# Optimization experiments

Hardware: AMD Instinct MI355X
Metric: run time of the kernel (lower is better)

## Reference

```python
import jax, jax.numpy as jnp
import numpy as np

B, SQ, SKV, H, D = 4, 128, 8192, 32, 128


def setup_inputs() -> dict:
    key = jax.random.key(0)
    k1, k2, k3 = jax.random.split(key, 3)
    q = jax.random.normal(k1, (B, SQ, H, D), dtype=jnp.float32)
    k = jax.random.normal(k2, (B, SKV, H, D), dtype=jnp.float32)
    v = jax.random.normal(k3, (B, SKV, H, D), dtype=jnp.float32)
    return {"q": q, "k": k, "v": v}


def reference(q, k, v):
    # Full (non-causal) multi-head decode attention with softmax scale 1/sqrt(D).
    # The kernel computes this via split-KV online softmax + LSE combine;
    # mathematically it equals standard softmax attention over all KV.
    scale = 1.0 / np.sqrt(q.shape[-1]).astype(np.float32)
    # scores: [B, H, SQ, SKV]
    scores = jnp.einsum("bqhd,bkhd->bhqk", q, k) * scale
    probs = jax.nn.softmax(scores, axis=-1)
    out = jnp.einsum("bhqk,bkhd->bqhd", probs, v)
    return out
```

## Files before the change

### kernel.cpp

```cpp
#include <hip/hip_runtime.h>
#include <hip/hip_bf16.h>
#include <cstdint>

#define B_ 4
#define SQ_ 128
#define SKV_ 8192
#define H_ 32
#define D_ 128
#define KT 32
#define HD (H_ * D_)

typedef __bf16 bf16x8 __attribute__((ext_vector_type(8)));
typedef float f32x4 __attribute__((ext_vector_type(4)));

union U4B8 { uint4 u; bf16x8 v; };

__device__ inline unsigned f2b_pack(float a, float b){
  unsigned ua = __float_as_uint(a); ua = (ua + 0x7FFFu + ((ua >> 16) & 1u)) >> 16;
  unsigned ub = __float_as_uint(b); ub = (ub + 0x7FFFu + ((ub >> 16) & 1u)) >> 16;
  return (ua & 0xFFFFu) | (ub << 16);
}
__device__ inline unsigned short f2b1(float a){
  unsigned ua = __float_as_uint(a);
  return (unsigned short)((ua + 0x7FFFu + ((ua >> 16) & 1u)) >> 16);
}

__global__ __launch_bounds__(512, 4) void mha_split_kernel(
    const float* __restrict__ q, const float* __restrict__ k, const float* __restrict__ v,
    float* __restrict__ Ubase, float* __restrict__ Lbase, float* __restrict__ outp, int nsplit)
{
  __shared__ char smem[40 * 1024] __attribute__((aligned(16)));

  const int tid = threadIdx.x;
  const int w = tid >> 6;
  const int l = tid & 63;
  const int g = l >> 4;
  const int c = l & 15;
  char* Plds = smem + 32768 + w * 1024;

  const int bh = blockIdx.x;
  const int split = blockIdx.y;
  const int b = bh >> 5, h = bh & 31;
  const int kps = SKV_ / nsplit;
  const int kv0 = split * kps;
  const int nt = kps / KT;

  const float qscale = 0.08838834764831845f * 1.4426950408889634f;

  bf16x8 qf[4];
  {
    const float* qr = q + (((size_t)b * SQ_ + (w * 16 + c)) * H_ + h) * D_;
#pragma unroll
    for (int ks = 0; ks < 4; ++ks) {
      int d0 = ks * 32 + g * 8;
      float4 x = *(const float4*)(qr + d0);
      float4 y = *(const float4*)(qr + d0 + 4);
      U4B8 t;
      t.u.x = f2b_pack(x.x * qscale, x.y * qscale);
      t.u.y = f2b_pack(x.z * qscale, x.w * qscale);
      t.u.z = f2b_pack(y.x * qscale, y.y * qscale);
      t.u.w = f2b_pack(y.z * qscale, y.w * qscale);
      qf[ks] = t.v;
    }
  }

  f32x4 oacc[8];
#pragma unroll
  for (int ni = 0; ni < 8; ++ni) oacc[ni] = (f32x4)0.0f;
  float lacc[4] = {};

  const float* kbase = k + ((size_t)b * SKV_ + kv0) * HD + (size_t)h * D_;
  const float* vbase = v + ((size_t)b * SKV_ + kv0) * HD + (size_t)h * D_;

  const int key_s = tid >> 4;
  const int d8_s  = (tid & 15) * 8;
  const int kp_s  = tid >> 5;
  const int d4_s  = (tid & 31) * 4;
  const int koff_w = key_s * 256 + ((d8_s * 2) ^ ((key_s & 7) << 4));

  float4 kreg0, kreg1, vreg0, vreg1;

  {
    const float* kt = kbase + (size_t)key_s * HD + d8_s;
    kreg0 = *(const float4*)(kt);
    kreg1 = *(const float4*)(kt + 4);
    const float* vt = vbase + (size_t)(kp_s * 2) * HD + d4_s;
    vreg0 = *(const float4*)(vt);
    vreg1 = *(const float4*)(vt + HD);
    uint4 kw;
    kw.x = f2b_pack(kreg0.x, kreg0.y); kw.y = f2b_pack(kreg0.z, kreg0.w);
    kw.z = f2b_pack(kreg1.x, kreg1.y); kw.w = f2b_pack(kreg1.z, kreg1.w);
    *(uint4*)(smem + koff_w) = kw;
    float va[4] = {vreg0.x, vreg0.y, vreg0.z, vreg0.w};
    float vb[4] = {vreg1.x, vreg1.y, vreg1.z, vreg1.w};
#pragma unroll
    for (int i = 0; i < 4; ++i) {
      int d = d4_s + i;
      int slot = ((kp_s >> 2) ^ ((d >> 2) & 3)) & 3;
      *(unsigned*)(smem + 16384 + d * 64 + slot * 16 + (kp_s & 3) * 4) = f2b_pack(va[i], vb[i]);
    }
  }
  __syncthreads();

  for (int t = 0; t < nt; ++t) {
    const int cur = t & 1;
    char* kc = smem + cur * 8192;
    char* vc = smem + 16384 + cur * 8192;

    if (t + 1 < nt) {
      const float* kt = kbase + (size_t)(t + 1) * KT * HD + (size_t)key_s * HD + d8_s;
      kreg0 = *(const float4*)(kt);
      kreg1 = *(const float4*)(kt + 4);
      const float* vt = vbase + (size_t)(t + 1) * KT * HD + (size_t)(kp_s * 2) * HD + d4_s;
      vreg0 = *(const float4*)(vt);
      vreg1 = *(const float4*)(vt + HD);
    }
    __builtin_amdgcn_sched_barrier(0);

    __builtin_amdgcn_s_setprio(1);
    f32x4 sacc[2];
#pragma unroll
    for (int ni = 0; ni < 2; ++ni) sacc[ni] = (f32x4)0.0f;
#pragma unroll
    for (int ni = 0; ni < 2; ++ni) {
      int key = ni * 16 + c;
      int rb = key * 256;
      int sw = (key & 7) << 4;
#pragma unroll
      for (int ks = 0; ks < 4; ++ks) {
        U4B8 bf;
        bf.u = *(uint4*)(kc + rb + ((ks * 64 + g * 16) ^ sw));
        sacc[ni] = __builtin_amdgcn_mfma_f32_16x16x32_bf16(qf[ks], bf.v, sacc[ni], 0, 0, 0);
      }
    }

#pragma unroll
    for (int ni = 0; ni < 2; ++ni) {
#pragma unroll
      for (int r = 0; r < 4; ++r) {
        float p = exp2f(sacc[ni][r]);
        lacc[r] += p;
        int row = g * 4 + r;
        int col = ni * 16 + c;
        int off = row * 64 + ((((col >> 3) ^ g) & 3) * 16) + (col & 7) * 2;
        *(unsigned short*)(Plds + off) = f2b1(p);
      }
    }

    {
      const int slot = ((g ^ (c >> 2)) & 3) * 16;
      U4B8 ap;
      ap.u = *(uint4*)(Plds + c * 64 + slot);
#pragma unroll
      for (int ni = 0; ni < 8; ++ni) {
        int d = ni * 16 + c;
        U4B8 bv;
        bv.u = *(uint4*)(vc + d * 64 + slot);
        oacc[ni] = __builtin_amdgcn_mfma_f32_16x16x32_bf16(ap.v, bv.v, oacc[ni], 0, 0, 0);
      }
    }
    __builtin_amdgcn_s_setprio(0);

    if (t + 1 < nt) {
      char* kn = smem + (cur ^ 1) * 8192;
      char* vn = smem + 16384 + (cur ^ 1) * 8192;
      uint4 kw;
      kw.x = f2b_pack(kreg0.x, kreg0.y); kw.y = f2b_pack(kreg0.z, kreg0.w);
      kw.z = f2b_pack(kreg1.x, kreg1.y); kw.w = f2b_pack(kreg1.z, kreg1.w);
      *(uint4*)(kn + koff_w) = kw;
      float va[4] = {vreg0.x, vreg0.y, vreg0.z, vreg0.w};
      float vb[4] = {vreg1.x, vreg1.y, vreg1.z, vreg1.w};
#pragma unroll
      for (int i = 0; i < 4; ++i) {
        int d = d4_s + i;
        int slot = ((kp_s >> 2) ^ ((d >> 2) & 3)) & 3;
        *(unsigned*)(vn + d * 64 + slot * 16 + (kp_s & 3) * 4) = f2b_pack(va[i], vb[i]);
      }
    }
    __syncthreads();
  }

#pragma unroll
  for (int r = 0; r < 4; ++r) {
    float s = lacc[r];
    s += __shfl_xor(s, 1, 16);
    s += __shfl_xor(s, 2, 16);
    s += __shfl_xor(s, 4, 16);
    s += __shfl_xor(s, 8, 16);
    lacc[r] = s;
  }

  if (nsplit == 1) {
    float* op = outp + (((size_t)b * SQ_) * H_ + h) * D_;
#pragma unroll
    for (int r = 0; r < 4; ++r) {
      int row = w * 16 + g * 4 + r;
      float inv = 1.0f / lacc[r];
#pragma unroll
      for (int ni = 0; ni < 8; ++ni) {
        op[(size_t)row * HD + ni * 16 + c] = oacc[ni][r] * inv;
      }
    }
  } else {
    float* Up = Ubase + ((size_t)split * 128 + bh) * (SQ_ * D_);
#pragma unroll
    for (int r = 0; r < 4; ++r) {
      int row = w * 16 + g * 4 + r;
#pragma unroll
      for (int ni = 0; ni < 8; ++ni) {
        Up[(size_t)row * D_ + ni * 16 + c] = oacc[ni][r];
      }
      if (c == 0) Lbase[((size_t)split * 128 + bh) * SQ_ + row] = lacc[r];
    }
  }
}

__global__ void mha_combine_kernel(const float* __restrict__ Ubase, const float* __restrict__ Lbase,
                                   float* __restrict__ outp, int nsplit) {
  int idx = blockIdx.x * 256 + threadIdx.x;
  int rowlin = idx >> 7;
  int d = idx & 127;
  float su = 0.f, sl = 0.f;
  for (int s = 0; s < nsplit; ++s) {
    su += Ubase[(size_t)s * (128 * SQ_ * D_) + idx];
    sl += Lbase[(size_t)s * (128 * SQ_) + rowlin];
  }
  int bh = rowlin >> 7, row = rowlin & 127;
  int b = bh >> 5, h = bh & 31;
  outp[(((size_t)b * SQ_ + row) * H_ + h) * D_ + d] = su / sl;
}

extern "C" void kernel_launch(void* const* d_in, const int* in_sizes, int n_in,
                              void* d_out, int out_size, void* d_ws, size_t ws_size,
                              hipStream_t stream) {
  const float* q = (const float*)d_in[0];
  const float* k = (const float*)d_in[1];
  const float* v = (const float*)d_in[2];
  float* outp = (float*)d_out;

  const size_t per_split = (size_t)128 * SQ_ * D_ * 4 + (size_t)128 * SQ_ * 4;
  int nsplit = 1;
  if (ws_size >= 4 * per_split) nsplit = 4;
  else if (ws_size >= 2 * per_split) nsplit = 2;

  float* Ubase = (float*)d_ws;
  float* Lbase = Ubase + (size_t)nsplit * 128 * SQ_ * D_;

  dim3 grid(128, nsplit);
  mha_split_kernel<<<grid, 512, 0, stream>>>(q, k, v, Ubase, Lbase, outp, nsplit);
  if (nsplit > 1) {
    mha_combine_kernel<<<(128 * SQ_ * D_) / 256, 256, 0, stream>>>(Ubase, Lbase, outp, nsplit);
  }
}
```

Measured before the change: 198.0 us.

## Deepen KV prefetch to two tiles ahead with unrolled ping-pong loop

Unrolls the KV tile loop by two and keeps two register sets of prefetched K/V, so global loads for tile t+2 are issued while tile t is computed, giving more latency hiding. Launch bounds minimum blocks per CU drops from 4 to 2 to allow the extra registers. It trades fewer resident waves (lower occupancy) for deeper software prefetch.

```diff
diff --git a/kernel.cpp b/kernel.cpp
--- a/kernel.cpp
+++ b/kernel.cpp
@@ -25,7 +25,7 @@
   return (unsigned short)((ua + 0x7FFFu + ((ua >> 16) & 1u)) >> 16);
 }
 
-__global__ __launch_bounds__(512, 4) void mha_split_kernel(
+__global__ __launch_bounds__(512, 2) void mha_split_kernel(
     const float* __restrict__ q, const float* __restrict__ k, const float* __restrict__ v,
     float* __restrict__ Ubase, float* __restrict__ Lbase, float* __restrict__ outp, int nsplit)
 {
@@ -78,107 +78,103 @@
   const int d4_s  = (tid & 31) * 4;
   const int koff_w = key_s * 256 + ((d8_s * 2) ^ ((key_s & 7) << 4));
 
-  float4 kreg0, kreg1, vreg0, vreg1;
-
-  {
-    const float* kt = kbase + (size_t)key_s * HD + d8_s;
-    kreg0 = *(const float4*)(kt);
-    kreg1 = *(const float4*)(kt + 4);
-    const float* vt = vbase + (size_t)(kp_s * 2) * HD + d4_s;
-    vreg0 = *(const float4*)(vt);
-    vreg1 = *(const float4*)(vt + HD);
-    uint4 kw;
-    kw.x = f2b_pack(kreg0.x, kreg0.y); kw.y = f2b_pack(kreg0.z, kreg0.w);
-    kw.z = f2b_pack(kreg1.x, kreg1.y); kw.w = f2b_pack(kreg1.z, kreg1.w);
-    *(uint4*)(smem + koff_w) = kw;
-    float va[4] = {vreg0.x, vreg0.y, vreg0.z, vreg0.w};
-    float vb[4] = {vreg1.x, vreg1.y, vreg1.z, vreg1.w};
-#pragma unroll
-    for (int i = 0; i < 4; ++i) {
-      int d = d4_s + i;
-      int slot = ((kp_s >> 2) ^ ((d >> 2) & 3)) & 3;
-      *(unsigned*)(smem + 16384 + d * 64 + slot * 16 + (kp_s & 3) * 4) = f2b_pack(va[i], vb[i]);
-    }
-  }
+  float4 kA0, kA1, vA0, vA1;
+  float4 kB0, kB1, vB0, vB1;
+
+#define ISSUE(T, K0r, K1r, V0r, V1r)                                          \
+  {                                                                           \
+    const float* kt_ = kbase + (size_t)(T) * KT * HD + (size_t)key_s * HD + d8_s; \
+    K0r = *(const float4*)(kt_);                                              \
+    K1r = *(const float4*)(kt_ + 4);                                          \
+    const float* vt_ = vbase + (size_t)(T) * KT * HD + (size_t)(kp_s * 2) * HD + d4_s; \
+    V0r = *(const float4*)(vt_);                                              \
+    V1r = *(const float4*)(vt_ + HD);                                         \
+  }
+
+#define WRITE_LDS(KDST, VDST, K0r, K1r, V0r, V1r)                             \
+  {                                                                           \
+    uint4 kw_;                                                                \
+    kw_.x = f2b_pack(K0r.x, K0r.y); kw_.y = f2b_pack(K0r.z, K0r.w);           \
+    kw_.z = f2b_pack(K1r.x, K1r.y); kw_.w = f2b_pack(K1r.z, K1r.w);           \
+    *(uint4*)((KDST) + koff_w) = kw_;                                         \
+    float va0_ = V0r.x, va1_ = V0r.y, va2_ = V0r.z, va3_ = V0r.w;             \
+    float vb0_ = V1r.x, vb1_ = V1r.y, vb2_ = V1r.z, vb3_ = V1r.w;             \
+    int d0_ = d4_s;                                                           \
+    int slotbase_ = (kp_s >> 2);                                              \
+    int s0_ = ((slotbase_ ^ ((d0_ >> 2) & 3)) & 3);                           \
+    *(unsigned*)((VDST) + (d0_ + 0) * 64 + s0_ * 16 + (kp_s & 3) * 4) = f2b_pack(va0_, vb0_); \
+    *(unsigned*)((VDST) + (d0_ + 1) * 64 + s0_ * 16 + (kp_s & 3) * 4) = f2b_pack(va1_, vb1_); \
+    *(unsigned*)((VDST) + (d0_ + 2) * 64 + s0_ * 16 + (kp_s & 3) * 4) = f2b_pack(va2_, vb2_); \
+    *(unsigned*)((VDST) + (d0_ + 3) * 64 + s0_ * 16 + (kp_s & 3) * 4) = f2b_pack(va3_, vb3_); \
+  }
+
+#define COMPUTE(KC, VC)                                                       \
+  {                                                                           \
+    __builtin_amdgcn_s_setprio(1);                                            \
+    f32x4 s0_ = (f32x4)0.0f, s1_ = (f32x4)0.0f;                               \
+    _Pragma("unroll")                                                         \
+    for (int ks = 0; ks < 4; ++ks) {                                          \
+      U4B8 bf0_, bf1_;                                                        \
+      int sw0_ = (c & 7) << 4;                                                \
+      bf0_.u = *(uint4*)((KC) + c * 256 + ((ks * 64 + g * 16) ^ sw0_));       \
+      int key1_ = 16 + c;                                                     \
+      bf1_.u = *(uint4*)((KC) + key1_ * 256 + ((ks * 64 + g * 16) ^ sw0_));   \
+      s0_ = __builtin_amdgcn_mfma_f32_16x16x32_bf16(qf[ks], bf0_.v, s0_, 0, 0, 0); \
+      s1_ = __builtin_amdgcn_mfma_f32_16x16x32_bf16(qf[ks], bf1_.v, s1_, 0, 0, 0); \
+    }                                                                         \
+    _Pragma("unroll")                                                         \
+    for (int r = 0; r < 4; ++r) {                                             \
+      float p0_ = exp2f(s0_[r]); lacc[r] += p0_;                              \
+      float p1_ = exp2f(s1_[r]); lacc[r] += p1_;                              \
+      int row_ = g * 4 + r;                                                   \
+      int col0_ = c, col1_ = 16 + c;                                          \
+      *(unsigned short*)(Plds + row_ * 64 + ((((col0_ >> 3) ^ g) & 3) * 16) + (col0_ & 7) * 2) = f2b1(p0_); \
+      *(unsigned short*)(Plds + row_ * 64 + ((((col1_ >> 3) ^ g) & 3) * 16) + (col1_ & 7) * 2) = f2b1(p1_); \
+    }                                                                         \
+    {                                                                         \
+      const int slot_ = ((g ^ (c >> 2)) & 3) * 16;                            \
+      U4B8 ap_;                                                               \
+      ap_.u = *(uint4*)(Plds + c * 64 + slot_);                               \
+      _Pragma("unroll")                                                       \
+      for (int ni = 0; ni < 8; ++ni) {                                        \
+        int d_ = ni * 16 + c;                                                 \
+        U4B8 bv_;                                                             \
+        bv_.u = *(uint4*)((VC) + d_ * 64 + slot_);                            \
+        oacc[ni] = __builtin_amdgcn_mfma_f32_16x16x32_bf16(ap_.v, bv_.v, oacc[ni], 0, 0, 0); \
+      }                                                                       \
+    }                                                                         \
+    __builtin_amdgcn_s_setprio(0);                                            \
+  }
+
+  char* const K0 = smem;
+  char* const K1 = smem + 8192;
+  char* const V0 = smem + 16384;
+  char* const V1 = smem + 24576;
+
+  ISSUE(0, kA0, kA1, vA0, vA1);
+  WRITE_LDS(K0, V0, kA0, kA1, vA0, vA1);
+  ISSUE(1, kA0, kA1, vA0, vA1);
   __syncthreads();
 
-  for (int t = 0; t < nt; ++t) {
-    const int cur = t & 1;
-    char* kc = smem + cur * 8192;
-    char* vc = smem + 16384 + cur * 8192;
-
-    if (t + 1 < nt) {
-      const float* kt = kbase + (size_t)(t + 1) * KT * HD + (size_t)key_s * HD + d8_s;
-      kreg0 = *(const float4*)(kt);
-      kreg1 = *(const float4*)(kt + 4);
-      const float* vt = vbase + (size_t)(t + 1) * KT * HD + (size_t)(kp_s * 2) * HD + d4_s;
-      vreg0 = *(const float4*)(vt);
-      vreg1 = *(const float4*)(vt + HD);
-    }
+  for (int tp = 0; tp < nt; tp += 2) {
+    if (tp + 2 < nt) ISSUE(tp + 2, kB0, kB1, vB0, vB1);
     __builtin_amdgcn_sched_barrier(0);
-
-    __builtin_amdgcn_s_setprio(1);
-    f32x4 sacc[2];
-#pragma unroll
-    for (int ni = 0; ni < 2; ++ni) sacc[ni] = (f32x4)0.0f;
-#pragma unroll
-    for (int ni = 0; ni < 2; ++ni) {
-      int key = ni * 16 + c;
-      int rb = key * 256;
-      int sw = (key & 7) << 4;
-#pragma unroll
-      for (int ks = 0; ks < 4; ++ks) {
-        U4B8 bf;
-        bf.u = *(uint4*)(kc + rb + ((ks * 64 + g * 16) ^ sw));
-        sacc[ni] = __builtin_amdgcn_mfma_f32_16x16x32_bf16(qf[ks], bf.v, sacc[ni], 0, 0, 0);
-      }
-    }
-
-#pragma unroll
-    for (int ni = 0; ni < 2; ++ni) {
-#pragma unroll
-      for (int r = 0; r < 4; ++r) {
-        float p = exp2f(sacc[ni][r]);
-        lacc[r] += p;
-        int row = g * 4 + r;
-        int col = ni * 16 + c;
-        int off = row * 64 + ((((col >> 3) ^ g) & 3) * 16) + (col & 7) * 2;
-        *(unsigned short*)(Plds + off) = f2b1(p);
-      }
-    }
-
-    {
-      const int slot = ((g ^ (c >> 2)) & 3) * 16;
-      U4B8 ap;
-      ap.u = *(uint4*)(Plds + c * 64 + slot);
-#pragma unroll
-      for (int ni = 0; ni < 8; ++ni) {
-        int d = ni * 16 + c;
-        U4B8 bv;
-        bv.u = *(uint4*)(vc + d * 64 + slot);
-        oacc[ni] = __builtin_amdgcn_mfma_f32_16x16x32_bf16(ap.v, bv.v, oacc[ni], 0, 0, 0);
-      }
-    }
-    __builtin_amdgcn_s_setprio(0);
-
-    if (t + 1 < nt) {
-      char* kn = smem + (cur ^ 1) * 8192;
-      char* vn = smem + 16384 + (cur ^ 1) * 8192;
-      uint4 kw;
-      kw.x = f2b_pack(kreg0.x, kreg0.y); kw.y = f2b_pack(kreg0.z, kreg0.w);
-      kw.z = f2b_pack(kreg1.x, kreg1.y); kw.w = f2b_pack(kreg1.z, kreg1.w);
-      *(uint4*)(kn + koff_w) = kw;
-      float va[4] = {vreg0.x, vreg0.y, vreg0.z, vreg0.w};
-      float vb[4] = {vreg1.x, vreg1.y, vreg1.z, vreg1.w};
-#pragma unroll
-      for (int i = 0; i < 4; ++i) {
-        int d = d4_s + i;
-        int slot = ((kp_s >> 2) ^ ((d >> 2) & 3)) & 3;
-        *(unsigned*)(vn + d * 64 + slot * 16 + (kp_s & 3) * 4) = f2b_pack(va[i], vb[i]);
-      }
-    }
+    COMPUTE(K0, V0);
+    WRITE_LDS(K1, V1, kA0, kA1, vA0, vA1);
     __syncthreads();
-  }
+
+    if (tp + 3 < nt) ISSUE(tp + 3, kA0, kA1, vA0, vA1);
+    __builtin_amdgcn_sched_barrier(0);
+    COMPUTE(K1, V1);
+    if (tp + 2 < nt) {
+      WRITE_LDS(K0, V0, kB0, kB1, vB0, vB1);
+    }
+    __syncthreads();
+  }
+
+#undef ISSUE
+#undef WRITE_LDS
+#undef COMPUTE
 
 #pragma unroll
   for (int r = 0; r < 4; ++r) {
```

Result: slower. 221.6 us (+11.9%).

## Fuse split-KV combine into attention kernel via last-block atomic counter

Applied to the files above, without the earlier changes.

Replaces the separate combine kernel with an in-kernel reduction: each split block atomically increments a per-(b,h) counter, and the last arriving block sums the partial outputs and LSE denominators and writes the final result with float4 stores. A tiny kernel zeroes the counters before the main launch. This removes the full-grid combine pass and moves the reduction into the tail of the attention kernel. In exchange it adds an extra small launch and serialises the reduction work onto one block per head. The split count is now hardcoded to 4, so the code assumes the workspace is large enough.

```diff
diff --git a/kernel.cpp b/kernel.cpp
--- a/kernel.cpp
+++ b/kernel.cpp
@@ -9,6 +9,7 @@
 #define D_ 128
 #define KT 32
 #define HD (H_ * D_)
+#define NSPLIT 4
 
 typedef __bf16 bf16x8 __attribute__((ext_vector_type(8)));
 typedef float f32x4 __attribute__((ext_vector_type(4)));
@@ -25,9 +26,12 @@
   return (unsigned short)((ua + 0x7FFFu + ((ua >> 16) & 1u)) >> 16);
 }
 
+__global__ void mha_zero_cnt(unsigned* cnt) { cnt[threadIdx.x] = 0; }
+
 __global__ __launch_bounds__(512, 4) void mha_split_kernel(
     const float* __restrict__ q, const float* __restrict__ k, const float* __restrict__ v,
-    float* __restrict__ Ubase, float* __restrict__ Lbase, float* __restrict__ outp, int nsplit)
+    float* __restrict__ Ubase, float* __restrict__ Lbase, unsigned* __restrict__ cnt,
+    float* __restrict__ outp)
 {
   __shared__ char smem[40 * 1024] __attribute__((aligned(16)));
 
@@ -41,7 +45,7 @@
   const int bh = blockIdx.x;
   const int split = blockIdx.y;
   const int b = bh >> 5, h = bh & 31;
-  const int kps = SKV_ / nsplit;
+  const int kps = SKV_ / NSPLIT;
   const int kv0 = split * kps;
   const int nt = kps / KT;
 
@@ -190,22 +194,11 @@
     lacc[r] = s;
   }
 
-  if (nsplit == 1) {
-    float* op = outp + (((size_t)b * SQ_) * H_ + h) * D_;
+  {
+    float* Up = Ubase + ((size_t)split * 128 + bh) * (SQ_ * D_);
 #pragma unroll
     for (int r = 0; r < 4; ++r) {
       int row = w * 16 + g * 4 + r;
-      float inv = 1.0f / lacc[r];
-#pragma unroll
-      for (int ni = 0; ni < 8; ++ni) {
-        op[(size_t)row * HD + ni * 16 + c] = oacc[ni][r] * inv;
-      }
-    }
-  } else {
-    float* Up = Ubase + ((size_t)split * 128 + bh) * (SQ_ * D_);
-#pragma unroll
-    for (int r = 0; r < 4; ++r) {
-      int row = w * 16 + g * 4 + r;
 #pragma unroll
       for (int ni = 0; ni < 8; ++ni) {
         Up[(size_t)row * D_ + ni * 16 + c] = oacc[ni][r];
@@ -213,21 +206,47 @@
       if (c == 0) Lbase[((size_t)split * 128 + bh) * SQ_ + row] = lacc[r];
     }
   }
-}
-
-__global__ void mha_combine_kernel(const float* __restrict__ Ubase, const float* __restrict__ Lbase,
-                                   float* __restrict__ outp, int nsplit) {
-  int idx = blockIdx.x * 256 + threadIdx.x;
-  int rowlin = idx >> 7;
-  int d = idx & 127;
-  float su = 0.f, sl = 0.f;
-  for (int s = 0; s < nsplit; ++s) {
-    su += Ubase[(size_t)s * (128 * SQ_ * D_) + idx];
-    sl += Lbase[(size_t)s * (128 * SQ_) + rowlin];
-  }
-  int bh = rowlin >> 7, row = rowlin & 127;
-  int b = bh >> 5, h = bh & 31;
-  outp[(((size_t)b * SQ_ + row) * H_ + h) * D_ + d] = su / sl;
+  __syncthreads();
+
+  volatile unsigned* flag = (volatile unsigned*)smem;
+  if (tid == 0) {
+    unsigned old = __hip_atomic_fetch_add(&cnt[bh], 1u, __ATOMIC_ACQ_REL,
+                                          __HIP_MEMORY_SCOPE_AGENT);
+    *flag = (old == NSPLIT - 1) ? 1u : 0u;
+  }
+  __syncthreads();
+  if (*flag == 0) return;
+
+  float* lsum = (float*)(smem + 64);
+  if (tid < 128) {
+    float s = 0.f;
+#pragma unroll
+    for (int sp = 0; sp < NSPLIT; ++sp)
+      s += Lbase[((size_t)sp * 128 + bh) * SQ_ + tid];
+    lsum[tid] = 1.0f / s;
+  }
+  __syncthreads();
+
+  {
+    const float4* U0 = (const float4*)(Ubase + ((size_t)0 * 128 + bh) * (SQ_ * D_));
+    const float4* U1 = (const float4*)(Ubase + ((size_t)1 * 128 + bh) * (SQ_ * D_));
+    const float4* U2 = (const float4*)(Ubase + ((size_t)2 * 128 + bh) * (SQ_ * D_));
+    const float4* U3 = (const float4*)(Ubase + ((size_t)3 * 128 + bh) * (SQ_ * D_));
+#pragma unroll
+    for (int it = 0; it < 8; ++it) {
+      int i = it * 512 + tid;
+      int row = i >> 5;
+      float4 a = U0[i], b4 = U1[i], c4 = U2[i], d4 = U3[i];
+      float inv = lsum[row];
+      float4 o;
+      o.x = (a.x + b4.x + c4.x + d4.x) * inv;
+      o.y = (a.y + b4.y + c4.y + d4.y) * inv;
+      o.z = (a.z + b4.z + c4.z + d4.z) * inv;
+      o.w = (a.w + b4.w + c4.w + d4.w) * inv;
+      int dcol = (i & 31) * 4;
+      *(float4*)(outp + (((size_t)b * SQ_ + row) * H_ + h) * D_ + dcol) = o;
+    }
+  }
 }
 
 extern "C" void kernel_launch(void* const* d_in, const int* in_sizes, int n_in,
@@ -238,17 +257,11 @@
   const float* v = (const float*)d_in[2];
   float* outp = (float*)d_out;
 
-  const size_t per_split = (size_t)128 * SQ_ * D_ * 4 + (size_t)128 * SQ_ * 4;
-  int nsplit = 1;
-  if (ws_size >= 4 * per_split) nsplit = 4;
-  else if (ws_size >= 2 * per_split) nsplit = 2;
-
   float* Ubase = (float*)d_ws;
-  float* Lbase = Ubase + (size_t)nsplit * 128 * SQ_ * D_;
-
-  dim3 grid(128, nsplit);
-  mha_split_kernel<<<grid, 512, 0, stream>>>(q, k, v, Ubase, Lbase, outp, nsplit);
-  if (nsplit > 1) {
-    mha_combine_kernel<<<(128 * SQ_ * D_) / 256, 256, 0, stream>>>(Ubase, Lbase, outp, nsplit);
-  }
-}
+  float* Lbase = Ubase + (size_t)NSPLIT * 128 * SQ_ * D_;
+  unsigned* cnt = (unsigned*)(Lbase + (size_t)NSPLIT * 128 * SQ_);
+
+  mha_zero_cnt<<<1, 128, 0, stream>>>(cnt);
+  dim3 grid(128, NSPLIT);
+  mha_split_kernel<<<grid, 512, 0, stream>>>(q, k, v, Ubase, Lbase, cnt, outp);
+}
```

Result: slower. 214.6 us (+8.4%).
